# Kernel optimization log

Hardware: AMD Instinct MI355X
Metric: run time of the kernel (lower is better)

## Reference

```python
import jax, jax.numpy as jnp
import numpy as np

N = 50000
E = 800000
G = 256          # number of graphs in the batch
F_IN = 128
H1, D1 = 12, 32  # conv1: heads, out-per-head (concat -> 384)
H2, D2 = 1, 64   # conv2: single head
NEG_SLOPE = 0.2


def setup_inputs() -> dict:
    key = jax.random.key(0)
    ks = jax.random.split(key, 12)
    x = jax.random.normal(ks[0], (N, F_IN), dtype=jnp.float32)
    edge_index = jax.random.randint(ks[1], (2, E), 0, N, dtype=jnp.int64)
    batch = jnp.sort(jax.random.randint(ks[2], (N,), 0, G, dtype=jnp.int64))
    # conv1 params (Glorot-ish scaling)
    W1 = jax.random.normal(ks[3], (F_IN, H1 * D1), dtype=jnp.float32) * (1.0 / np.sqrt(F_IN))
    att_src1 = jax.random.normal(ks[4], (H1, D1), dtype=jnp.float32) * (1.0 / np.sqrt(D1))
    att_dst1 = jax.random.normal(ks[5], (H1, D1), dtype=jnp.float32) * (1.0 / np.sqrt(D1))
    bias1 = jnp.zeros((H1 * D1,), dtype=jnp.float32)
    # conv2 params
    W2 = jax.random.normal(ks[6], (H1 * D1, H2 * D2), dtype=jnp.float32) * (1.0 / np.sqrt(H1 * D1))
    att_src2 = jax.random.normal(ks[7], (H2, D2), dtype=jnp.float32) * (1.0 / np.sqrt(D2))
    att_dst2 = jax.random.normal(ks[8], (H2, D2), dtype=jnp.float32) * (1.0 / np.sqrt(D2))
    bias2 = jnp.zeros((H2 * D2,), dtype=jnp.float32)
    return {"x": x, "edge_index": edge_index, "batch": batch,
            "W1": W1, "att_src1": att_src1, "att_dst1": att_dst1, "bias1": bias1,
            "W2": W2, "att_src2": att_src2, "att_dst2": att_dst2, "bias2": bias2}


def gat_conv(x, src, dst, W, att_src, att_dst, bias, heads, d_out):
    # x: [N, F] -> h: [N, heads, d_out]
    h = (x @ W).reshape(N, heads, d_out)
    # per-node attention halves: [N, heads]
    a_src = jnp.einsum('nhd,hd->nh', h, att_src)
    a_dst = jnp.einsum('nhd,hd->nh', h, att_dst)
    # per-edge logits (edges include self-loops): [Etot, heads]
    e = jax.nn.leaky_relu(a_src[src] + a_dst[dst], NEG_SLOPE)
    # segment softmax over incoming edges of each destination node
    m = jax.ops.segment_max(e, dst, num_segments=N)          # [N, heads]
    e = jnp.exp(e - m[dst])
    s = jax.ops.segment_sum(e, dst, num_segments=N)          # [N, heads]
    alpha = e / s[dst]
    # weighted aggregation: [N, heads, d_out]
    out = jax.ops.segment_sum(alpha[:, :, None] * h[src], dst, num_segments=N)
    return out.reshape(N, heads * d_out) + bias


def reference(x, edge_index, batch, W1, att_src1, att_dst1, bias1,
              W2, att_src2, att_dst2, bias2):
    # add self-loops (PyG GATConv default add_self_loops=True)
    loops = jnp.arange(N, dtype=edge_index.dtype)
    src = jnp.concatenate([edge_index[0], loops])
    dst = jnp.concatenate([edge_index[1], loops])

    h = jax.nn.relu(gat_conv(x, src, dst, W1, att_src1, att_dst1, bias1, H1, D1))
    h = gat_conv(h, src, dst, W2, att_src2, att_dst2, bias2, H2, D2)

    # global mean pool over graphs
    sums = jax.ops.segment_sum(h, batch, num_segments=G)                 # [G, 64]
    cnts = jax.ops.segment_sum(jnp.ones((N,), h.dtype), batch, num_segments=G)
    return sums / jnp.maximum(cnts, 1.0)[:, None]
```

## Files before the change

### kernel.cpp

```cpp
#include <hip/hip_runtime.h>

#define N_NODES 50000
#define N_EDGES 800000
#define ETOT (N_EDGES + N_NODES)
#define G_GRAPHS 256
#define F_IN 128
#define H1 12
#define D1 32
#define C1 (H1*D1)
#define C2 64
#define NEG 0.2f
#define SCAN_B 1024
#define NBLK_SCAN ((N_NODES + SCAN_B - 1)/SCAN_B)

using bf16x8  = __attribute__((ext_vector_type(8))) short;
using ushort8 = __attribute__((ext_vector_type(8))) unsigned short;
using f32x4   = __attribute__((ext_vector_type(4))) float;

__device__ __forceinline__ float lrelu(float x){ return x > 0.f ? x : NEG*x; }
__device__ __forceinline__ unsigned short f2bf(float f){
  unsigned u = __float_as_uint(f);
  u += 0x7fffu + ((u >> 16) & 1u);
  return (unsigned short)(u >> 16);
}
__device__ __forceinline__ float bf2f(unsigned short h){
  return __uint_as_float(((unsigned)h) << 16);
}

__global__ void cast_x_kernel(const float* __restrict__ x, unsigned short* __restrict__ xb){
  int i = blockIdx.x*blockDim.x + threadIdx.x;
  int base = i*4;
  if (base >= N_NODES*F_IN) return;
  float4 v = *(const float4*)(x + base);
  ushort4 o; o.x=f2bf(v.x); o.y=f2bf(v.y); o.z=f2bf(v.z); o.w=f2bf(v.w);
  *(ushort4*)(xb + base) = o;
}
__global__ void transpose_w_kernel(const float* __restrict__ W, unsigned short* __restrict__ Wt,
                                   int K, int Nc){
  int i = blockIdx.x*blockDim.x + threadIdx.x;
  if (i >= K*Nc) return;
  int n = i / K, k = i % K;
  Wt[i] = f2bf(W[(size_t)k*Nc + n]);
}
__global__ void wab_prep(const float* __restrict__ W1, const float* __restrict__ att_src,
                         const float* __restrict__ att_dst, unsigned short* __restrict__ wAb){
  int i = blockIdx.x*blockDim.x + threadIdx.x;
  if (i >= 32*F_IN) return;
  int c = i >> 7, k = i & 127;
  float v = 0.f;
  if (c < 12){
    #pragma unroll
    for (int dd=0; dd<D1; ++dd) v += W1[(size_t)k*C1 + c*D1 + dd] * att_src[c*D1 + dd];
  } else if (c < 24){
    int h = c - 12;
    #pragma unroll
    for (int dd=0; dd<D1; ++dd) v += W1[(size_t)k*C1 + h*D1 + dd] * att_dst[h*D1 + dd];
  }
  wAb[i] = f2bf(v);
}

template<int BM,int BN,int WM,int WN,bool F32OUT>
__global__ __launch_bounds__(256) void gemm_mfma(const unsigned short* __restrict__ A,
    const unsigned short* __restrict__ Bt, void* __restrict__ Cv,
    int M, int N, int K){
  constexpr int BK = 32;
  __shared__ unsigned short As2[4][BM][8];
  __shared__ unsigned short Bs2[4][BN][8];
  const int tid  = threadIdx.x;
  const int wid  = tid >> 6, lane = tid & 63;
  constexpr int NWX = BN / WN;
  const int wrow = (wid / NWX) * WM, wcol = (wid % NWX) * WN;
  constexpr int MR = WM/16, NR = WN/16;
  const int row0 = blockIdx.x * BM, col0 = blockIdx.y * BN;
  const int r = lane & 15, koct = lane >> 4;
  f32x4 acc[MR][NR];
  #pragma unroll
  for (int m=0;m<MR;m++)
    #pragma unroll
    for (int n=0;n<NR;n++) acc[m][n] = f32x4{0.f,0.f,0.f,0.f};

  for (int k0 = 0; k0 < K; k0 += BK){
    for (int s = tid; s < BM*8; s += 256){
      int rr = s >> 3, cc = (s & 7) * 4;
      int gr = row0 + rr;
      ushort4 v = (gr < M) ? *(const ushort4*)(A + (size_t)gr*K + k0 + cc)
                           : ushort4{0,0,0,0};
      *(ushort4*)(&As2[cc>>3][rr][cc&7]) = v;
    }
    for (int s = tid; s < BN*8; s += 256){
      int rr = s >> 3, cc = (s & 7) * 4;
      ushort4 v = *(const ushort4*)(Bt + (size_t)(col0+rr)*K + k0 + cc);
      *(ushort4*)(&Bs2[cc>>3][rr][cc&7]) = v;
    }
    __syncthreads();
    bf16x8 af[MR], bq[NR];
    #pragma unroll
    for (int m=0;m<MR;m++) af[m] = *(const bf16x8*)(&As2[koct][wrow + m*16 + r][0]);
    #pragma unroll
    for (int n=0;n<NR;n++) bq[n] = *(const bf16x8*)(&Bs2[koct][wcol + n*16 + r][0]);
    #pragma unroll
    for (int m=0;m<MR;m++)
      #pragma unroll
      for (int n=0;n<NR;n++)
        acc[m][n] = __builtin_amdgcn_mfma_f32_16x16x32_bf16(af[m], bq[n], acc[m][n], 0,0,0);
    __syncthreads();
  }
  #pragma unroll
  for (int m=0;m<MR;m++){
    #pragma unroll
    for (int rr=0; rr<4; rr++){
      int grow = row0 + wrow + m*16 + koct*4 + rr;
      if (grow < M){
        #pragma unroll
        for (int n=0;n<NR;n++){
          if constexpr (F32OUT)
            ((float*)Cv)[(size_t)grow*N + col0 + wcol + n*16 + r] = acc[m][n][rr];
          else
            ((unsigned short*)Cv)[(size_t)grow*N + col0 + wcol + n*16 + r] = f2bf(acc[m][n][rr]);
        }
      }
    }
  }
}

__global__ void count_kernel(const int* __restrict__ ei, int* __restrict__ counts){
  int e = blockIdx.x*blockDim.x + threadIdx.x;
  if (e >= ETOT) return;
  int d = (e < N_EDGES) ? ei[N_EDGES + e] : (e - N_EDGES);
  atomicAdd(&counts[d], 1);
}
__global__ __launch_bounds__(SCAN_B) void scan_pass1(const int* __restrict__ counts,
    int* __restrict__ excl, int* __restrict__ bsum){
  __shared__ int sdata[SCAN_B];
  int i = blockIdx.x*SCAN_B + threadIdx.x;
  int v = (i < N_NODES) ? counts[i] : 0;
  sdata[threadIdx.x] = v;
  __syncthreads();
  for (int off=1; off<SCAN_B; off<<=1){
    int t = (threadIdx.x >= off) ? sdata[threadIdx.x-off] : 0;
    __syncthreads();
    sdata[threadIdx.x] += t;
    __syncthreads();
  }
  if (i < N_NODES) excl[i] = sdata[threadIdx.x] - v;
  if (threadIdx.x == SCAN_B-1) bsum[blockIdx.x] = sdata[SCAN_B-1];
}
__global__ void scan_pass2(int* __restrict__ bsum){
  if (threadIdx.x == 0){
    int acc = 0;
    for (int b=0;b<NBLK_SCAN;b++){ int t = bsum[b]; bsum[b] = acc; acc += t; }
  }
}
__global__ void scan_pass3(int* __restrict__ rowptr, const int* __restrict__ bsum,
                           int* __restrict__ cursor){
  int i = blockIdx.x*blockDim.x + threadIdx.x;
  if (i < N_NODES){
    int r = rowptr[i] + bsum[i/SCAN_B];
    rowptr[i] = r; cursor[i] = r;
  }
  if (i == N_NODES) rowptr[N_NODES] = ETOT;
}
__global__ void scatter_kernel(const int* __restrict__ ei, int* __restrict__ cursor,
                               int* __restrict__ csr_src){
  int e = blockIdx.x*blockDim.x + threadIdx.x;
  if (e >= ETOT) return;
  int s, d;
  if (e < N_EDGES){ s = ei[e]; d = ei[N_EDGES + e]; } else { s = d = e - N_EDGES; }
  int slot = atomicAdd(&cursor[d], 1);
  csr_src[slot] = s;
}

__global__ __launch_bounds__(64) void alpha1_kernel(const int* __restrict__ rowptr,
    const int* __restrict__ csr, const float* __restrict__ asd,
    float* __restrict__ alpha){
  int d = blockIdx.x, lane = threadIdx.x;
  int r0 = rowptr[d], r1 = rowptr[d+1], deg = r1 - r0;
  float4 ad0 = *(const float4*)(asd + (size_t)d*32 + 12);
  float4 ad1 = *(const float4*)(asd + (size_t)d*32 + 16);
  float4 ad2 = *(const float4*)(asd + (size_t)d*32 + 20);
  float ad[12] = {ad0.x,ad0.y,ad0.z,ad0.w, ad1.x,ad1.y,ad1.z,ad1.w, ad2.x,ad2.y,ad2.z,ad2.w};

  if (deg <= 64){
    bool act = lane < deg;
    int j = r0 + lane;
    int s = act ? csr[j] : 0;
    float4 s0 = *(const float4*)(asd + (size_t)s*32);
    float4 s1 = *(const float4*)(asd + (size_t)s*32 + 4);
    float4 s2 = *(const float4*)(asd + (size_t)s*32 + 8);
    float as[12] = {s0.x,s0.y,s0.z,s0.w, s1.x,s1.y,s1.z,s1.w, s2.x,s2.y,s2.z,s2.w};
    float w[12];
    #pragma unroll
    for (int h=0; h<12; ++h){
      float l = act ? lrelu(as[h] + ad[h]) : -1e30f;
      float m = l;
      #pragma unroll
      for (int off=32; off; off>>=1) m = fmaxf(m, __shfl_xor(m, off));
      float wv = act ? __expf(l - m) : 0.f;
      float ss = wv;
      #pragma unroll
      for (int off=32; off; off>>=1) ss += __shfl_xor(ss, off);
      w[h] = wv / ss;
    }
    if (act){
      float4 o0 = {w[0],w[1],w[2],w[3]};
      float4 o1 = {w[4],w[5],w[6],w[7]};
      float4 o2 = {w[8],w[9],w[10],w[11]};
      *(float4*)(alpha + (size_t)j*12)     = o0;
      *(float4*)(alpha + (size_t)j*12 + 4) = o1;
      *(float4*)(alpha + (size_t)j*12 + 8) = o2;
    }
  } else {
    float mx[12], ss[12];
    #pragma unroll
    for (int h=0;h<12;h++){ mx[h] = -1e30f; ss[h] = 0.f; }
    for (int j = r0 + lane; j < r1; j += 64){
      int s = csr[j];
      float4 s0 = *(const float4*)(asd + (size_t)s*32);
      float4 s1 = *(const float4*)(asd + (size_t)s*32 + 4);
      float4 s2 = *(const float4*)(asd + (size_t)s*32 + 8);
      float as[12] = {s0.x,s0.y,s0.z,s0.w, s1.x,s1.y,s1.z,s1.w, s2.x,s2.y,s2.z,s2.w};
      #pragma unroll
      for (int h=0;h<12;h++) mx[h] = fmaxf(mx[h], lrelu(as[h] + ad[h]));
    }
    #pragma unroll
    for (int h=0;h<12;h++){
      #pragma unroll
      for (int off=32; off; off>>=1) mx[h] = fmaxf(mx[h], __shfl_xor(mx[h], off));
    }
    for (int j = r0 + lane; j < r1; j += 64){
      int s = csr[j];
      float4 s0 = *(const float4*)(asd + (size_t)s*32);
      float4 s1 = *(const float4*)(asd + (size_t)s*32 + 4);
      float4 s2 = *(const float4*)(asd + (size_t)s*32 + 8);
      float as[12] = {s0.x,s0.y,s0.z,s0.w, s1.x,s1.y,s1.z,s1.w, s2.x,s2.y,s2.z,s2.w};
      float w[12];
      #pragma unroll
      for (int h=0;h<12;h++){ w[h] = __expf(lrelu(as[h]+ad[h]) - mx[h]); ss[h] += w[h]; }
      float4 o0 = {w[0],w[1],w[2],w[3]};
      float4 o1 = {w[4],w[5],w[6],w[7]};
      float4 o2 = {w[8],w[9],w[10],w[11]};
      *(float4*)(alpha + (size_t)j*12)     = o0;
      *(float4*)(alpha + (size_t)j*12 + 4) = o1;
      *(float4*)(alpha + (size_t)j*12 + 8) = o2;
    }
    float inv[12];
    #pragma unroll
    for (int h=0;h<12;h++){
      #pragma unroll
      for (int off=32; off; off>>=1) ss[h] += __shfl_xor(ss[h], off);
      inv[h] = 1.f / ss[h];
    }
    for (int j = r0 + lane; j < r1; j += 64){
      float4 o0 = *(const float4*)(alpha + (size_t)j*12);
      float4 o1 = *(const float4*)(alpha + (size_t)j*12 + 4);
      float4 o2 = *(const float4*)(alpha + (size_t)j*12 + 8);
      o0.x*=inv[0]; o0.y*=inv[1]; o0.z*=inv[2]; o0.w*=inv[3];
      o1.x*=inv[4]; o1.y*=inv[5]; o1.z*=inv[6]; o1.w*=inv[7];
      o2.x*=inv[8]; o2.y*=inv[9]; o2.z*=inv[10]; o2.w*=inv[11];
      *(float4*)(alpha + (size_t)j*12)     = o0;
      *(float4*)(alpha + (size_t)j*12 + 4) = o1;
      *(float4*)(alpha + (size_t)j*12 + 8) = o2;
    }
  }
}

__global__ __launch_bounds__(64) void alpha2_kernel(const int* __restrict__ rowptr,
    const int* __restrict__ csr, const float* __restrict__ asrc,
    const float* __restrict__ adst, float* __restrict__ alpha){
  int d = blockIdx.x, lane = threadIdx.x;
  int r0 = rowptr[d], r1 = rowptr[d+1], deg = r1 - r0;
  float ad = adst[d];
  if (deg <= 64){
    bool act = lane < deg;
    int j = r0 + lane;
    int s = act ? csr[j] : 0;
    float l = act ? lrelu(asrc[s] + ad) : -1e30f;
    float m = l;
    #pragma unroll
    for (int off=32; off; off>>=1) m = fmaxf(m, __shfl_xor(m, off));
    float wv = act ? __expf(l - m) : 0.f;
    float ss = wv;
    #pragma unroll
    for (int off=32; off; off>>=1) ss += __shfl_xor(ss, off);
    if (act) alpha[j] = wv / ss;
  } else {
    float mx = -1e30f, ss = 0.f;
    for (int j = r0 + lane; j < r1; j += 64){
      int s = csr[j];
      mx = fmaxf(mx, lrelu(asrc[s] + ad));
    }
    #pragma unroll
    for (int off=32; off; off>>=1) mx = fmaxf(mx, __shfl_xor(mx, off));
    for (int j = r0 + lane; j < r1; j += 64){
      int s = csr[j];
      float w = __expf(lrelu(asrc[s] + ad) - mx);
      ss += w; alpha[j] = w;
    }
    #pragma unroll
    for (int off=32; off; off>>=1) ss += __shfl_xor(ss, off);
    float inv = 1.f / ss;
    for (int j = r0 + lane; j < r1; j += 64)
      alpha[j] *= inv;
  }
}

__global__ __launch_bounds__(256) void agg1x_kernel(const int* __restrict__ rowptr,
    const int* __restrict__ csr, const unsigned short* __restrict__ xb,
    const float* __restrict__ alpha, const unsigned short* __restrict__ w1t,
    const float* __restrict__ bias, unsigned short* __restrict__ out1){
  constexpr int ROWE = H1*F_IN + 8;
  __shared__ unsigned short agg[16*ROWE];
  int tid = threadIdx.x;
  int g = tid >> 4, t16 = tid & 15;
  int d = blockIdx.x*16 + g;
  int r0 = rowptr[d], r1 = rowptr[d+1];
  float acc[12][8];
  #pragma unroll
  for (int h=0;h<12;h++)
    #pragma unroll
    for (int i=0;i<8;i++) acc[h][i] = 0.f;

  float4 a0={0,0,0,0}, a1={0,0,0,0}, a2={0,0,0,0};
  ushort8 xv = {0,0,0,0,0,0,0,0};
  if (r0 < r1){
    int s = csr[r0];
    a0 = *(const float4*)(alpha + (size_t)r0*12);
    a1 = *(const float4*)(alpha + (size_t)r0*12 + 4);
    a2 = *(const float4*)(alpha + (size_t)r0*12 + 8);
    xv = *(const ushort8*)(xb + (size_t)s*F_IN + t16*8);
  }
  for (int j = r0; j < r1; ++j){
    float4 c0=a0, c1=a1, c2=a2; ushort8 cx=xv;
    if (j+1 < r1){
      int s = csr[j+1];
      a0 = *(const float4*)(alpha + (size_t)(j+1)*12);
      a1 = *(const float4*)(alpha + (size_t)(j+1)*12 + 4);
      a2 = *(const float4*)(alpha + (size_t)(j+1)*12 + 8);
      xv = *(const ushort8*)(xb + (size_t)s*F_IN + t16*8);
    }
    float xf[8];
    #pragma unroll
    for (int i=0;i<8;i++) xf[i] = bf2f((unsigned short)cx[i]);
    float aw[12] = {c0.x,c0.y,c0.z,c0.w, c1.x,c1.y,c1.z,c1.w, c2.x,c2.y,c2.z,c2.w};
    #pragma unroll
    for (int h=0;h<12;h++)
      #pragma unroll
      for (int i=0;i<8;i++) acc[h][i] += aw[h]*xf[i];
  }
  #pragma unroll
  for (int h=0;h<12;h++){
    ushort8 v;
    #pragma unroll
    for (int i=0;i<8;i++) v[i] = f2bf(acc[h][i]);
    *(ushort8*)(&agg[g*ROWE + h*F_IN + t16*8]) = v;
  }
  __syncthreads();
  int wid = tid >> 6, lane = tid & 63;
  int r = lane & 15, q = lane >> 4;
  for (int hh = 0; hh < 3; ++hh){
    int h = wid*3 + hh;
    #pragma unroll
    for (int nb=0; nb<2; ++nb){
      f32x4 c = {0.f,0.f,0.f,0.f};
      #pragma unroll
      for (int kk=0; kk<4; ++kk){
        bf16x8 af = *(const bf16x8*)(&agg[r*ROWE + h*F_IN + kk*32 + q*8]);
        bf16x8 bq = *(const bf16x8*)(w1t + (size_t)(h*32 + nb*16 + r)*F_IN + kk*32 + q*8);
        c = __builtin_amdgcn_mfma_f32_16x16x32_bf16(af, bq, c, 0,0,0);
      }
      int col = h*32 + nb*16 + r;
      float bv = bias[col];
      #pragma unroll
      for (int rr=0; rr<4; ++rr){
        int drow = q*4 + rr;
        int od = blockIdx.x*16 + drow;
        float v = fmaxf(c[rr] + bv, 0.f);
        out1[(size_t)od*C1 + col] = f2bf(v);
      }
    }
  }
}

__global__ void a2_kernel(const unsigned short* __restrict__ h2,
    const float* __restrict__ att_src, const float* __restrict__ att_dst,
    float* __restrict__ a_src, float* __restrict__ a_dst){
  int n = blockIdx.x*blockDim.x + threadIdx.x;
  if (n >= N_NODES) return;
  const unsigned short* hp = h2 + (size_t)n*C2;
  float s=0.f, d=0.f;
  #pragma unroll
  for (int k4=0;k4<16;k4++){
    ushort4 v = *(const ushort4*)(hp + k4*4);
    int b = k4*4;
    s += bf2f(v.x)*att_src[b] + bf2f(v.y)*att_src[b+1] + bf2f(v.z)*att_src[b+2] + bf2f(v.w)*att_src[b+3];
    d += bf2f(v.x)*att_dst[b] + bf2f(v.y)*att_dst[b+1] + bf2f(v.z)*att_dst[b+2] + bf2f(v.w)*att_dst[b+3];
  }
  a_src[n]=s; a_dst[n]=d;
}

#define AGG2_CH 64
__global__ __launch_bounds__(64) void agg2_pool(const int* __restrict__ rowptr,
    const int* __restrict__ csr, const unsigned short* __restrict__ h2,
    const float* __restrict__ alpha, const float* __restrict__ bias,
    const int* __restrict__ batch, float* __restrict__ pool){
  int d = blockIdx.x, tid = threadIdx.x;
  int r0 = rowptr[d], r1 = rowptr[d+1];
  __shared__ float w_lds[AGG2_CH];
  __shared__ int   s_lds[AGG2_CH];
  __shared__ float red[3][C2];
  int grp = tid >> 4;
  int fb  = (tid & 15) * 4;
  float a0=0.f, a1=0.f, a2=0.f, a3=0.f;
  for (int c0 = r0; c0 < r1; c0 += AGG2_CH){
    int nc = min(AGG2_CH, r1 - c0);
    __syncthreads();
    if (tid < nc){ w_lds[tid] = alpha[c0 + tid]; s_lds[tid] = csr[c0 + tid]; }
    __syncthreads();
    for (int e = grp; e < nc; e += 4){
      int s = s_lds[e];
      float w = w_lds[e];
      ushort4 hv = *(const ushort4*)(h2 + (size_t)s*C2 + fb);
      a0 += w*bf2f(hv.x); a1 += w*bf2f(hv.y); a2 += w*bf2f(hv.z); a3 += w*bf2f(hv.w);
    }
  }
  __syncthreads();
  if (grp > 0){
    float* p = &red[grp-1][fb];
    p[0]=a0; p[1]=a1; p[2]=a2; p[3]=a3;
  }
  __syncthreads();
  if (grp == 0){
    int g = batch[d];
    float4 b4 = *(const float4*)(bias + fb);
    float v0 = a0 + red[0][fb+0] + red[1][fb+0] + red[2][fb+0] + b4.x;
    float v1 = a1 + red[0][fb+1] + red[1][fb+1] + red[2][fb+1] + b4.y;
    float v2 = a2 + red[0][fb+2] + red[1][fb+2] + red[2][fb+2] + b4.z;
    float v3 = a3 + red[0][fb+3] + red[1][fb+3] + red[2][fb+3] + b4.w;
    atomicAdd(&pool[g*C2 + fb+0], v0);
    atomicAdd(&pool[g*C2 + fb+1], v1);
    atomicAdd(&pool[g*C2 + fb+2], v2);
    atomicAdd(&pool[g*C2 + fb+3], v3);
  }
}

__global__ void cnt_kernel(const int* __restrict__ batch, int* __restrict__ cnt){
  int n = blockIdx.x*blockDim.x + threadIdx.x;
  if (n < N_NODES) atomicAdd(&cnt[batch[n]], 1);
}
__global__ void finalize_kernel(const float* __restrict__ sums, const int* __restrict__ cnt,
                                float* __restrict__ out){
  int i = blockIdx.x*blockDim.x + threadIdx.x;
  if (i >= G_GRAPHS*C2) return;
  int g = i >> 6;
  out[i] = sums[i] / fmaxf((float)cnt[g], 1.f);
}

extern "C" void kernel_launch(void* const* d_in, const int* in_sizes, int n_in,
                              void* d_out, int out_size, void* d_ws, size_t ws_size,
                              hipStream_t stream) {
  const float* x        = (const float*)d_in[0];
  const int*   ei       = (const int*)  d_in[1];
  const int*   batch    = (const int*)  d_in[2];
  const float* W1       = (const float*)d_in[3];
  const float* att_src1 = (const float*)d_in[4];
  const float* att_dst1 = (const float*)d_in[5];
  const float* bias1    = (const float*)d_in[6];
  const float* W2       = (const float*)d_in[7];
  const float* att_src2 = (const float*)d_in[8];
  const float* att_dst2 = (const float*)d_in[9];
  const float* bias2    = (const float*)d_in[10];
  float* out = (float*)d_out;

  char* ws = (char*)d_ws;
  size_t o = 0;
  auto alloc = [&](size_t bytes)->size_t{ size_t r=o; o=(o+bytes+255)&~(size_t)255; return r; };

  size_t xb_o     = alloc((size_t)N_NODES*F_IN*2);
  size_t w1t_o    = alloc((size_t)C1*F_IN*2);
  size_t w2t_o    = alloc((size_t)C2*C1*2);
  size_t wab_o    = alloc((size_t)32*F_IN*2);
  size_t asd_o    = alloc((size_t)N_NODES*32*4);
  size_t out1_o   = alloc((size_t)N_NODES*C1*2);
  size_t h2_o     = alloc((size_t)N_NODES*C2*2);
  size_t asrc2_o  = alloc((size_t)N_NODES*4);
  size_t adst2_o  = alloc((size_t)N_NODES*4);
  size_t alpha1_o = alloc((size_t)ETOT*H1*4);
  size_t alpha2_o = alloc((size_t)ETOT*4);
  size_t zero_beg = o;
  size_t counts_o = alloc((size_t)N_NODES*4);
  size_t pool_o   = alloc((size_t)G_GRAPHS*C2*4);
  size_t cnt_o    = alloc((size_t)G_GRAPHS*4);
  size_t zero_end = o;
  size_t rowptr_o = alloc((size_t)(N_NODES+1)*4);
  size_t bsum_o   = alloc((size_t)NBLK_SCAN*4);
  size_t cursor_o = alloc((size_t)N_NODES*4);
  size_t csr_o    = alloc((size_t)ETOT*4);

  unsigned short* xb    = (unsigned short*)(ws + xb_o);
  unsigned short* w1t   = (unsigned short*)(ws + w1t_o);
  unsigned short* w2t   = (unsigned short*)(ws + w2t_o);
  unsigned short* wab   = (unsigned short*)(ws + wab_o);
  float* asd    = (float*)(ws + asd_o);
  unsigned short* out1b = (unsigned short*)(ws + out1_o);
  unsigned short* h2b   = (unsigned short*)(ws + h2_o);
  float* asrc2  = (float*)(ws + asrc2_o);
  float* adst2  = (float*)(ws + adst2_o);
  float* alpha1 = (float*)(ws + alpha1_o);
  float* alpha2 = (float*)(ws + alpha2_o);
  int*   counts = (int*)  (ws + counts_o);
  float* poolf  = (float*)(ws + pool_o);
  int*   cnt    = (int*)  (ws + cnt_o);
  int*   rowptr = (int*)  (ws + rowptr_o);
  int*   bsum   = (int*)  (ws + bsum_o);
  int*   cursor = (int*)  (ws + cursor_o);
  int*   csrsrc = (int*)  (ws + csr_o);

  hipMemsetAsync(ws + zero_beg, 0, zero_end - zero_beg, stream);

  const int TPB = 256;
  int egrid = (ETOT + TPB - 1)/TPB;

  cast_x_kernel<<<(N_NODES*F_IN/4 + TPB-1)/TPB, TPB, 0, stream>>>(x, xb);
  transpose_w_kernel<<<(F_IN*C1 + TPB-1)/TPB, TPB, 0, stream>>>(W1, w1t, F_IN, C1);
  transpose_w_kernel<<<(C1*C2 + TPB-1)/TPB, TPB, 0, stream>>>(W2, w2t, C1, C2);
  wab_prep<<<(32*F_IN + TPB-1)/TPB, TPB, 0, stream>>>(W1, att_src1, att_dst1, wab);

  count_kernel<<<egrid, TPB, 0, stream>>>(ei, counts);
  scan_pass1<<<NBLK_SCAN, SCAN_B, 0, stream>>>(counts, rowptr, bsum);
  scan_pass2<<<1, 64, 0, stream>>>(bsum);
  scan_pass3<<<(N_NODES + TPB)/TPB, TPB, 0, stream>>>(rowptr, bsum, cursor);
  scatter_kernel<<<egrid, TPB, 0, stream>>>(ei, cursor, csrsrc);

  gemm_mfma<128,32,32,32,true><<<dim3((N_NODES+127)/128, 1), 256, 0, stream>>>(xb, wab, asd, N_NODES, 32, F_IN);
  alpha1_kernel<<<N_NODES, 64, 0, stream>>>(rowptr, csrsrc, asd, alpha1);
  agg1x_kernel<<<N_NODES/16, 256, 0, stream>>>(rowptr, csrsrc, xb, alpha1, w1t, bias1, out1b);

  gemm_mfma<128,64,64,32,false><<<dim3((N_NODES+127)/128, 1), 256, 0, stream>>>(out1b, w2t, h2b, N_NODES, C2, C1);
  a2_kernel<<<(N_NODES + TPB-1)/TPB, TPB, 0, stream>>>(h2b, att_src2, att_dst2, asrc2, adst2);
  alpha2_kernel<<<N_NODES, 64, 0, stream>>>(rowptr, csrsrc, asrc2, adst2, alpha2);
  agg2_pool<<<N_NODES, 64, 0, stream>>>(rowptr, csrsrc, h2b, alpha2, bias2, batch, poolf);

  cnt_kernel<<<(N_NODES + TPB-1)/TPB, TPB, 0, stream>>>(batch, cnt);
  finalize_kernel<<<(G_GRAPHS*C2 + TPB-1)/TPB, TPB, 0, stream>>>(poolf, cnt, out);
}
```

Baseline: 510.4 us.

## Fuse layer-2 softmax into aggregation and halve agg1x shared memory

Removes the separate alpha2 kernel. The aggregation kernel now computes an online max/sum softmax over incoming edges and recomputes each edge weight on the fly, which drops the alpha2 buffer write and read and one launch. Separately, agg1x stages its 12 heads through shared memory in two halves of 6, roughly halving LDS use per block to raise occupancy, at the cost of an extra barrier. The fused kernel reads csr/asrc twice and does more exp work per edge.

```diff
diff --git a/kernel.cpp b/kernel.cpp
--- a/kernel.cpp
+++ b/kernel.cpp
@@ -264,51 +264,11 @@
   }
 }
 
-__global__ __launch_bounds__(64) void alpha2_kernel(const int* __restrict__ rowptr,
-    const int* __restrict__ csr, const float* __restrict__ asrc,
-    const float* __restrict__ adst, float* __restrict__ alpha){
-  int d = blockIdx.x, lane = threadIdx.x;
-  int r0 = rowptr[d], r1 = rowptr[d+1], deg = r1 - r0;
-  float ad = adst[d];
-  if (deg <= 64){
-    bool act = lane < deg;
-    int j = r0 + lane;
-    int s = act ? csr[j] : 0;
-    float l = act ? lrelu(asrc[s] + ad) : -1e30f;
-    float m = l;
-    #pragma unroll
-    for (int off=32; off; off>>=1) m = fmaxf(m, __shfl_xor(m, off));
-    float wv = act ? __expf(l - m) : 0.f;
-    float ss = wv;
-    #pragma unroll
-    for (int off=32; off; off>>=1) ss += __shfl_xor(ss, off);
-    if (act) alpha[j] = wv / ss;
-  } else {
-    float mx = -1e30f, ss = 0.f;
-    for (int j = r0 + lane; j < r1; j += 64){
-      int s = csr[j];
-      mx = fmaxf(mx, lrelu(asrc[s] + ad));
-    }
-    #pragma unroll
-    for (int off=32; off; off>>=1) mx = fmaxf(mx, __shfl_xor(mx, off));
-    for (int j = r0 + lane; j < r1; j += 64){
-      int s = csr[j];
-      float w = __expf(lrelu(asrc[s] + ad) - mx);
-      ss += w; alpha[j] = w;
-    }
-    #pragma unroll
-    for (int off=32; off; off>>=1) ss += __shfl_xor(ss, off);
-    float inv = 1.f / ss;
-    for (int j = r0 + lane; j < r1; j += 64)
-      alpha[j] *= inv;
-  }
-}
-
 __global__ __launch_bounds__(256) void agg1x_kernel(const int* __restrict__ rowptr,
     const int* __restrict__ csr, const unsigned short* __restrict__ xb,
     const float* __restrict__ alpha, const unsigned short* __restrict__ w1t,
     const float* __restrict__ bias, unsigned short* __restrict__ out1){
-  constexpr int ROWE = H1*F_IN + 8;
+  constexpr int ROWE = 6*F_IN + 8;
   __shared__ unsigned short agg[16*ROWE];
   int tid = threadIdx.x;
   int g = tid >> 4, t16 = tid & 15;
@@ -347,35 +307,36 @@
       #pragma unroll
       for (int i=0;i<8;i++) acc[h][i] += aw[h]*xf[i];
   }
-  #pragma unroll
-  for (int h=0;h<12;h++){
-    ushort8 v;
-    #pragma unroll
-    for (int i=0;i<8;i++) v[i] = f2bf(acc[h][i]);
-    *(ushort8*)(&agg[g*ROWE + h*F_IN + t16*8]) = v;
-  }
-  __syncthreads();
+
   int wid = tid >> 6, lane = tid & 63;
   int r = lane & 15, q = lane >> 4;
-  for (int hh = 0; hh < 3; ++hh){
-    int h = wid*3 + hh;
-    #pragma unroll
-    for (int nb=0; nb<2; ++nb){
+  #pragma unroll
+  for (int half = 0; half < 2; ++half){
+    if (half) __syncthreads();
+    #pragma unroll
+    for (int h = 0; h < 6; ++h){
+      ushort8 v;
+      #pragma unroll
+      for (int i=0;i<8;i++) v[i] = f2bf(acc[half*6+h][i]);
+      *(ushort8*)(&agg[g*ROWE + h*F_IN + t16*8]) = v;
+    }
+    __syncthreads();
+    for (int t = wid; t < 12; t += 4){
+      int h = t >> 1, nb = t & 1;
+      int hh = half*6 + h;
       f32x4 c = {0.f,0.f,0.f,0.f};
       #pragma unroll
       for (int kk=0; kk<4; ++kk){
         bf16x8 af = *(const bf16x8*)(&agg[r*ROWE + h*F_IN + kk*32 + q*8]);
-        bf16x8 bq = *(const bf16x8*)(w1t + (size_t)(h*32 + nb*16 + r)*F_IN + kk*32 + q*8);
+        bf16x8 bq = *(const bf16x8*)(w1t + (size_t)(hh*32 + nb*16 + r)*F_IN + kk*32 + q*8);
         c = __builtin_amdgcn_mfma_f32_16x16x32_bf16(af, bq, c, 0,0,0);
       }
-      int col = h*32 + nb*16 + r;
+      int col = hh*32 + nb*16 + r;
       float bv = bias[col];
       #pragma unroll
       for (int rr=0; rr<4; ++rr){
-        int drow = q*4 + rr;
-        int od = blockIdx.x*16 + drow;
-        float v = fmaxf(c[rr] + bv, 0.f);
-        out1[(size_t)od*C1 + col] = f2bf(v);
+        int od = blockIdx.x*16 + q*4 + rr;
+        out1[(size_t)od*C1 + col] = f2bf(fmaxf(c[rr] + bv, 0.f));
       }
     }
   }
@@ -399,13 +360,30 @@
 }
 
 #define AGG2_CH 64
-__global__ __launch_bounds__(64) void agg2_pool(const int* __restrict__ rowptr,
+__global__ __launch_bounds__(64) void agg2f_kernel(const int* __restrict__ rowptr,
     const int* __restrict__ csr, const unsigned short* __restrict__ h2,
-    const float* __restrict__ alpha, const float* __restrict__ bias,
-    const int* __restrict__ batch, float* __restrict__ pool){
+    const float* __restrict__ asrc, const float* __restrict__ adst,
+    const float* __restrict__ bias, const int* __restrict__ batch,
+    float* __restrict__ pool){
   int d = blockIdx.x, tid = threadIdx.x;
   int r0 = rowptr[d], r1 = rowptr[d+1];
-  __shared__ float w_lds[AGG2_CH];
+  float ad = adst[d];
+  float m = -1e30f, ss = 0.f;
+  for (int j = r0 + tid; j < r1; j += 64){
+    float l = lrelu(asrc[csr[j]] + ad);
+    float mn = fmaxf(m, l);
+    ss = ss*__expf(m - mn) + __expf(l - mn);
+    m = mn;
+  }
+  #pragma unroll
+  for (int off=32; off; off>>=1){
+    float m2 = __shfl_xor(m, off);
+    float s2 = __shfl_xor(ss, off);
+    float mn = fmaxf(m, m2);
+    ss = ss*__expf(m - mn) + s2*__expf(m2 - mn);
+    m = mn;
+  }
+  float inv = 1.f / ss;
   __shared__ int   s_lds[AGG2_CH];
   __shared__ float red[3][C2];
   int grp = tid >> 4;
@@ -414,11 +392,11 @@
   for (int c0 = r0; c0 < r1; c0 += AGG2_CH){
     int nc = min(AGG2_CH, r1 - c0);
     __syncthreads();
-    if (tid < nc){ w_lds[tid] = alpha[c0 + tid]; s_lds[tid] = csr[c0 + tid]; }
+    if (tid < nc) s_lds[tid] = csr[c0 + tid];
     __syncthreads();
     for (int e = grp; e < nc; e += 4){
       int s = s_lds[e];
-      float w = w_lds[e];
+      float w = __expf(lrelu(asrc[s] + ad) - m);
       ushort4 hv = *(const ushort4*)(h2 + (size_t)s*C2 + fb);
       a0 += w*bf2f(hv.x); a1 += w*bf2f(hv.y); a2 += w*bf2f(hv.z); a3 += w*bf2f(hv.w);
     }
@@ -432,10 +410,10 @@
   if (grp == 0){
     int g = batch[d];
     float4 b4 = *(const float4*)(bias + fb);
-    float v0 = a0 + red[0][fb+0] + red[1][fb+0] + red[2][fb+0] + b4.x;
-    float v1 = a1 + red[0][fb+1] + red[1][fb+1] + red[2][fb+1] + b4.y;
-    float v2 = a2 + red[0][fb+2] + red[1][fb+2] + red[2][fb+2] + b4.z;
-    float v3 = a3 + red[0][fb+3] + red[1][fb+3] + red[2][fb+3] + b4.w;
+    float v0 = (a0 + red[0][fb+0] + red[1][fb+0] + red[2][fb+0])*inv + b4.x;
+    float v1 = (a1 + red[0][fb+1] + red[1][fb+1] + red[2][fb+1])*inv + b4.y;
+    float v2 = (a2 + red[0][fb+2] + red[1][fb+2] + red[2][fb+2])*inv + b4.z;
+    float v3 = (a3 + red[0][fb+3] + red[1][fb+3] + red[2][fb+3])*inv + b4.w;
     atomicAdd(&pool[g*C2 + fb+0], v0);
     atomicAdd(&pool[g*C2 + fb+1], v1);
     atomicAdd(&pool[g*C2 + fb+2], v2);
@@ -485,7 +463,6 @@
   size_t asrc2_o  = alloc((size_t)N_NODES*4);
   size_t adst2_o  = alloc((size_t)N_NODES*4);
   size_t alpha1_o = alloc((size_t)ETOT*H1*4);
-  size_t alpha2_o = alloc((size_t)ETOT*4);
   size_t zero_beg = o;
   size_t counts_o = alloc((size_t)N_NODES*4);
   size_t pool_o   = alloc((size_t)G_GRAPHS*C2*4);
@@ -506,7 +483,6 @@
   float* asrc2  = (float*)(ws + asrc2_o);
   float* adst2  = (float*)(ws + adst2_o);
   float* alpha1 = (float*)(ws + alpha1_o);
-  float* alpha2 = (float*)(ws + alpha2_o);
   int*   counts = (int*)  (ws + counts_o);
   float* poolf  = (float*)(ws + pool_o);
   int*   cnt    = (int*)  (ws + cnt_o);
@@ -537,8 +513,7 @@
 
   gemm_mfma<128,64,64,32,false><<<dim3((N_NODES+127)/128, 1), 256, 0, stream>>>(out1b, w2t, h2b, N_NODES, C2, C1);
   a2_kernel<<<(N_NODES + TPB-1)/TPB, TPB, 0, stream>>>(h2b, att_src2, att_dst2, asrc2, adst2);
-  alpha2_kernel<<<N_NODES, 64, 0, stream>>>(rowptr, csrsrc, asrc2, adst2, alpha2);
-  agg2_pool<<<N_NODES, 64, 0, stream>>>(rowptr, csrsrc, h2b, alpha2, bias2, batch, poolf);
+  agg2f_kernel<<<N_NODES, 64, 0, stream>>>(rowptr, csrsrc, h2b, asrc2, adst2, bias2, batch, poolf);
 
   cnt_kernel<<<(N_NODES + TPB-1)/TPB, TPB, 0, stream>>>(batch, cnt);
   finalize_kernel<<<(G_GRAPHS*C2 + TPB-1)/TPB, TPB, 0, stream>>>(poolf, cnt, out);
```

After: 510.2 us. Within noise of the previous version (-0.0%).
